# Kernel tuning notes

Measured on AMD Instinct MI355X. Metric: run time of the kernel, lower is better.

The kernel has to match this reference:

```python
import jax, jax.numpy as jnp
import numpy as np

B, NQ, NK = 4, 2048, 2048
QDIM = CDIM = 1024
H, DH = 16, 64  # heads, dim_head; inner_dim = H*DH = 1024
SCALE = DH ** -0.5
WSTD = 0.02


def setup_inputs() -> dict:
    key = jax.random.key(0)
    ks = jax.random.split(key, 6)
    inner = H * DH
    return {
        "x": jax.random.normal(ks[0], (B, NQ, QDIM), dtype=jnp.float32),
        "context": jax.random.normal(ks[1], (B, NK, CDIM), dtype=jnp.float32),
        "Wq": jax.random.normal(ks[2], (inner, QDIM), dtype=jnp.float32) * WSTD,
        "Wk": jax.random.normal(ks[3], (inner, CDIM), dtype=jnp.float32) * WSTD,
        "Wv": jax.random.normal(ks[4], (inner, CDIM), dtype=jnp.float32) * WSTD,
        "Wo": jax.random.normal(ks[5], (QDIM, inner), dtype=jnp.float32) * WSTD,
        "bo": jnp.zeros((QDIM,), dtype=jnp.float32),
    }


def reference(x, context, Wq, Wk, Wv, Wo, bo):
    b, nq, _ = x.shape
    nk = context.shape[1]
    # Linear projections (torch Linear: y = x @ W.T)
    q = (x @ Wq.T).reshape(b, nq, H, DH)        # b n h d
    k = (context @ Wk.T).reshape(b, nk, H, DH)
    v = (context @ Wv.T).reshape(b, nk, H, DH)
    # sim = Q K^T * scale, materialized as in the original einsum
    sim = jnp.einsum('bihd,bjhd->bhij', q, k) * SCALE
    attn = jax.nn.softmax(sim, axis=-1)
    out = jnp.einsum('bhij,bjhd->bihd', attn, v).reshape(b, nq, H * DH)
    return out @ Wo.T + bo
```

## Files before the change

### kernel.cpp

```cpp
#include <hip/hip_runtime.h>
#include <cstdint>
#include <cstddef>


typedef __attribute__((ext_vector_type(8))) short short8;
typedef __attribute__((ext_vector_type(4))) float f32x4;
typedef __attribute__((ext_vector_type(4))) unsigned short ushort4v;

#define GLD16(gsrc, ldst) \
  __builtin_amdgcn_global_load_lds((const __attribute__((address_space(1))) unsigned int*)(gsrc), \
                                   (__attribute__((address_space(3))) unsigned int*)(ldst), 16, 0, 0)

__device__ __forceinline__ unsigned short f32_to_bf16(float f) {
  unsigned int u = __builtin_bit_cast(unsigned int, f);
  u += 0x7FFFu + ((u >> 16) & 1u);
  return (unsigned short)(u >> 16);
}

__device__ __forceinline__ unsigned int pack2_bf16(float lo, float hi) {
  return (unsigned int)f32_to_bf16(lo) | ((unsigned int)f32_to_bf16(hi) << 16);
}

__global__ __launch_bounds__(256) void cvt_bf16(const float* __restrict__ in,
                                                unsigned short* __restrict__ out,
                                                int n4, float scale) {
  int i = blockIdx.x * 256 + threadIdx.x;
  const int stride = gridDim.x * 256;
  for (; i < n4; i += stride) {
    float4 v = reinterpret_cast<const float4*>(in)[i];
    ushort4v o;
    o.x = f32_to_bf16(v.x * scale);
    o.y = f32_to_bf16(v.y * scale);
    o.z = f32_to_bf16(v.z * scale);
    o.w = f32_to_bf16(v.w * scale);
    reinterpret_cast<ushort4v*>(out)[i] = o;
  }
}

template<bool BF16_OUT, bool BIAS>
__global__ __launch_bounds__(256) void gemm_bt(const unsigned short* __restrict__ A,
                                               const unsigned short* __restrict__ Bm,
                                               void* __restrict__ Cout,
                                               const float* __restrict__ bias,
                                               int M, int N, int K) {
  __shared__ __align__(16) unsigned short smA[128 * 32];
  __shared__ __align__(16) unsigned short smB[128 * 32];

  const int t    = threadIdx.x;
  const int lane = t & 63;
  const int wid  = t >> 6;
  const int l15  = lane & 15;
  const int l16  = lane >> 4;
  const int m0   = blockIdx.y * 128;
  const int n0   = blockIdx.x * 128;
  const int wr   = (wid >> 1) * 64;
  const int wc   = (wid & 1) * 64;

  f32x4 acc[4][4];
#pragma unroll
  for (int i = 0; i < 4; ++i)
#pragma unroll
    for (int j = 0; j < 4; ++j) acc[i][j] = (f32x4){0.f, 0.f, 0.f, 0.f};

  const char* Abase = (const char*)A + (size_t)m0 * K * 2;
  const char* Bbase = (const char*)Bm + (size_t)n0 * K * 2;

  for (int k0 = 0; k0 < K; k0 += 32) {
#pragma unroll
    for (int i = 0; i < 2; ++i) {
      int g = i * 256 + t;
      int r = g >> 2, c = g & 3;
      int cs = c ^ ((r >> 1) & 3);
      const char* srcA = Abase + (size_t)r * (K * 2) + (size_t)k0 * 2 + cs * 16;
      const char* srcB = Bbase + (size_t)r * (K * 2) + (size_t)k0 * 2 + cs * 16;
      char* dA = (char*)smA + (g & ~63) * 16;
      char* dB = (char*)smB + (g & ~63) * 16;
      GLD16(srcA, dA);
      GLD16(srcB, dB);
    }
    __syncthreads();

    short8 af[4], bfv[4];
#pragma unroll
    for (int mi = 0; mi < 4; ++mi) {
      int row = wr + mi * 16 + l15;
      int cs = l16 ^ ((row >> 1) & 3);
      af[mi] = *reinterpret_cast<const short8*>((const char*)smA + row * 64 + cs * 16);
    }
#pragma unroll
    for (int ni = 0; ni < 4; ++ni) {
      int row = wc + ni * 16 + l15;
      int cs = l16 ^ ((row >> 1) & 3);
      bfv[ni] = *reinterpret_cast<const short8*>((const char*)smB + row * 64 + cs * 16);
    }
#pragma unroll
    for (int mi = 0; mi < 4; ++mi)
#pragma unroll
      for (int ni = 0; ni < 4; ++ni)
        acc[mi][ni] = __builtin_amdgcn_mfma_f32_16x16x32_bf16(af[mi], bfv[ni], acc[mi][ni], 0, 0, 0);
    __syncthreads();
  }

#pragma unroll
  for (int mi = 0; mi < 4; ++mi)
#pragma unroll
    for (int ni = 0; ni < 4; ++ni)
#pragma unroll
      for (int r = 0; r < 4; ++r) {
        int row = m0 + wr + mi * 16 + l16 * 4 + r;
        int col = n0 + wc + ni * 16 + l15;
        float v = acc[mi][ni][r];
        if (BIAS) v += bias[col];
        if (BF16_OUT)
          ((unsigned short*)Cout)[(size_t)row * N + col] = f32_to_bf16(v);
        else
          ((float*)Cout)[(size_t)row * N + col] = v;
      }
}

__global__ __launch_bounds__(256, 3) void flash_attn(const unsigned short* __restrict__ Q,
                                                     const unsigned short* __restrict__ Kb,
                                                     const unsigned short* __restrict__ Vt,
                                                     unsigned short* __restrict__ O) {
  __shared__ __align__(16) unsigned short smK[2][64 * 64];
  __shared__ __align__(16) unsigned short smV[2][64 * 64];
  __shared__ __align__(16) unsigned int   smP[4][32 * 36];

  const int t    = threadIdx.x;
  const int lane = t & 63;
  const int wid  = t >> 6;
  const int l15  = lane & 15;
  const int l16  = lane >> 4;
  const int qt   = blockIdx.x;
  const int h    = blockIdx.y;
  const int b    = blockIdx.z;

  const char* Kbase = (const char*)Kb + ((size_t)(b * 2048) * 1024 + h * 64) * 2;
  const char* Vbase = (const char*)Vt + ((size_t)(h * 64) * 8192 + b * 2048) * 2;
  unsigned int* smPw = &smP[wid][0];

  short8 qf[2][2];
#pragma unroll
  for (int qg = 0; qg < 2; ++qg)
#pragma unroll
    for (int kk = 0; kk < 2; ++kk) {
      size_t idx = (size_t)(b * 2048 + qt * 128 + wid * 32 + qg * 16 + l15) * 1024
                 + (size_t)h * 64 + kk * 32 + l16 * 8;
      qf[qg][kk] = *reinterpret_cast<const short8*>(&Q[idx]);
    }
  asm volatile("s_waitcnt vmcnt(0)" ::: "memory");
  __builtin_amdgcn_sched_barrier(0);

  auto stage = [&](int buf, int j0) {
#pragma unroll
    for (int i = 0; i < 2; ++i) {
      int g = i * 256 + t;
      int r = g >> 3, c = g & 7;
      int cs = c ^ (r & 7);
      const char* srcK = Kbase + (size_t)(j0 + r) * 2048 + cs * 16;
      const char* srcV = Vbase + (size_t)r * 16384 + (size_t)j0 * 2 + cs * 16;
      GLD16(srcK, (char*)&smK[buf][0] + (g & ~63) * 16);
      GLD16(srcV, (char*)&smV[buf][0] + (g & ~63) * 16);
    }
  };

  f32x4 accO[2][4];
  float m_run[2], l_run[2];
#pragma unroll
  for (int qg = 0; qg < 2; ++qg) {
    m_run[qg] = -1.0e30f;
    l_run[qg] = 0.f;
#pragma unroll
    for (int di = 0; di < 4; ++di) accO[qg][di] = (f32x4){0.f, 0.f, 0.f, 0.f};
  }

  stage(0, 0);

  for (int jt = 0; jt < 32; ++jt) {
    const int buf = jt & 1;
    if (jt < 31) {
      stage(buf ^ 1, (jt + 1) * 64);
      asm volatile("s_waitcnt vmcnt(4)" ::: "memory");
    } else {
      asm volatile("s_waitcnt vmcnt(0)" ::: "memory");
    }
    __builtin_amdgcn_sched_barrier(0);
    __builtin_amdgcn_s_barrier();

    short8 kf[4][2];
#pragma unroll
    for (int kc = 0; kc < 4; ++kc)
#pragma unroll
      for (int kk = 0; kk < 2; ++kk) {
        int row = kc * 16 + l15;
        int cs = (kk * 4 + l16) ^ (row & 7);
        kf[kc][kk] = *reinterpret_cast<const short8*>((const char*)&smK[buf][0] + row * 128 + cs * 16);
      }
    f32x4 s[2][4];
    const f32x4 z = (f32x4){0.f, 0.f, 0.f, 0.f};
    __builtin_amdgcn_s_setprio(1);
#pragma unroll
    for (int qg = 0; qg < 2; ++qg)
#pragma unroll
      for (int kc = 0; kc < 4; ++kc) {
        f32x4 tmp = __builtin_amdgcn_mfma_f32_16x16x32_bf16(kf[kc][0], qf[qg][0], z, 0, 0, 0);
        s[qg][kc] = __builtin_amdgcn_mfma_f32_16x16x32_bf16(kf[kc][1], qf[qg][1], tmp, 0, 0, 0);
      }
    __builtin_amdgcn_s_setprio(0);

    short8 vf[4][2];
#pragma unroll
    for (int di = 0; di < 4; ++di)
#pragma unroll
      for (int kk = 0; kk < 2; ++kk) {
        int row = di * 16 + l15;
        int cs = (kk * 4 + l16) ^ (row & 7);
        vf[di][kk] = *reinterpret_cast<const short8*>((const char*)&smV[buf][0] + row * 128 + cs * 16);
      }

#pragma unroll
    for (int qg = 0; qg < 2; ++qg) {
      float vmax = s[qg][0][0];
#pragma unroll
      for (int kc = 0; kc < 4; ++kc)
#pragma unroll
        for (int r = 0; r < 4; ++r) vmax = fmaxf(vmax, s[qg][kc][r]);
      vmax = fmaxf(vmax, __shfl_xor(vmax, 16));
      vmax = fmaxf(vmax, __shfl_xor(vmax, 32));

      if (__any(vmax > m_run[qg] + 8.0f)) {
        float mnew = fmaxf(m_run[qg], vmax);
        float alpha = __expf(m_run[qg] - mnew);
        m_run[qg] = mnew;
        l_run[qg] *= alpha;
        int av = __builtin_bit_cast(int, alpha);
#pragma unroll
        for (int r = 0; r < 4; ++r) {
          float at = __builtin_bit_cast(float, __builtin_amdgcn_ds_bpermute((l16 * 4 + r) * 4, av));
#pragma unroll
          for (int di = 0; di < 4; ++di) accO[qg][di][r] *= at;
        }
      }

      float rsum = 0.f;
#pragma unroll
      for (int kc = 0; kc < 4; ++kc)
#pragma unroll
        for (int r = 0; r < 4; ++r) {
          float p = __expf(s[qg][kc][r] - m_run[qg]);
          s[qg][kc][r] = p;
          rsum += p;
        }
      rsum += __shfl_xor(rsum, 16);
      rsum += __shfl_xor(rsum, 32);
      l_run[qg] += rsum;

#pragma unroll
      for (int kc = 0; kc < 4; ++kc) {
        unsigned int w0 = pack2_bf16(s[qg][kc][0], s[qg][kc][1]);
        unsigned int w1 = pack2_bf16(s[qg][kc][2], s[qg][kc][3]);
        int word = (qg * 16 + l15) * 36 + kc * 8 + l16 * 2;
        *reinterpret_cast<uint2*>(&smPw[word]) = uint2{w0, w1};
      }
    }

    asm volatile("s_waitcnt lgkmcnt(0)" ::: "memory");
    __builtin_amdgcn_sched_barrier(0);

    short8 pf[2][2];
#pragma unroll
    for (int qg = 0; qg < 2; ++qg)
#pragma unroll
      for (int kk = 0; kk < 2; ++kk) {
        int word = (qg * 16 + l15) * 36 + kk * 16 + l16 * 4;
        pf[qg][kk] = *reinterpret_cast<const short8*>(&smPw[word]);
      }

    __builtin_amdgcn_s_setprio(1);
#pragma unroll
    for (int qg = 0; qg < 2; ++qg)
#pragma unroll
      for (int di = 0; di < 4; ++di) {
        accO[qg][di] = __builtin_amdgcn_mfma_f32_16x16x32_bf16(pf[qg][0], vf[di][0], accO[qg][di], 0, 0, 0);
        accO[qg][di] = __builtin_amdgcn_mfma_f32_16x16x32_bf16(pf[qg][1], vf[di][1], accO[qg][di], 0, 0, 0);
      }
    __builtin_amdgcn_s_setprio(0);

    __builtin_amdgcn_s_barrier();
  }

#pragma unroll
  for (int qg = 0; qg < 2; ++qg) {
    float inv = 1.f / l_run[qg];
    int iv = __builtin_bit_cast(int, inv);
#pragma unroll
    for (int r = 0; r < 4; ++r) {
      float it = __builtin_bit_cast(float, __builtin_amdgcn_ds_bpermute((l16 * 4 + r) * 4, iv));
      int row = b * 2048 + qt * 128 + wid * 32 + qg * 16 + l16 * 4 + r;
#pragma unroll
      for (int di = 0; di < 4; ++di) {
        int col = h * 64 + di * 16 + l15;
        O[(size_t)row * 1024 + col] = f32_to_bf16(accO[qg][di][r] * it);
      }
    }
  }
}

extern "C" void kernel_launch(void* const* d_in, const int* in_sizes, int n_in,
                              void* d_out, int out_size, void* d_ws, size_t ws_size,
                              hipStream_t stream) {
  (void)in_sizes; (void)n_in; (void)out_size; (void)ws_size;
  const float* x   = (const float*)d_in[0];
  const float* ctx = (const float*)d_in[1];
  const float* Wq  = (const float*)d_in[2];
  const float* Wk  = (const float*)d_in[3];
  const float* Wv  = (const float*)d_in[4];
  const float* Wo  = (const float*)d_in[5];
  const float* bo  = (const float*)d_in[6];
  float* out = (float*)d_out;

  char* ws = (char*)d_ws;
  const size_t MB = 1024 * 1024;
  unsigned short* xb  = (unsigned short*)(ws + 0);
  unsigned short* cb  = (unsigned short*)(ws + 16 * MB);
  unsigned short* Qb  = (unsigned short*)(ws + 32 * MB);
  unsigned short* Kb  = (unsigned short*)(ws + 48 * MB);
  unsigned short* Vtb = (unsigned short*)(ws + 64 * MB);
  unsigned short* wqb = (unsigned short*)(ws + 80 * MB);
  unsigned short* wkb = (unsigned short*)(ws + 82 * MB);
  unsigned short* wvb = (unsigned short*)(ws + 84 * MB);
  unsigned short* wob = (unsigned short*)(ws + 86 * MB);
  unsigned short* Ob  = xb;

  const float SCALE = 0.125f;

  cvt_bf16<<<2048, 256, 0, stream>>>(x,   xb,  (4*2048*1024)/4, 1.0f);
  cvt_bf16<<<2048, 256, 0, stream>>>(ctx, cb,  (4*2048*1024)/4, 1.0f);
  cvt_bf16<<<1024, 256, 0, stream>>>(Wq,  wqb, (1024*1024)/4, SCALE);
  cvt_bf16<<<1024, 256, 0, stream>>>(Wk,  wkb, (1024*1024)/4, 1.0f);
  cvt_bf16<<<1024, 256, 0, stream>>>(Wv,  wvb, (1024*1024)/4, 1.0f);
  cvt_bf16<<<1024, 256, 0, stream>>>(Wo,  wob, (1024*1024)/4, 1.0f);

  gemm_bt<true, false><<<dim3(1024/128, 8192/128), 256, 0, stream>>>(xb, wqb, Qb, nullptr, 8192, 1024, 1024);
  gemm_bt<true, false><<<dim3(1024/128, 8192/128), 256, 0, stream>>>(cb, wkb, Kb, nullptr, 8192, 1024, 1024);
  gemm_bt<true, false><<<dim3(8192/128, 1024/128), 256, 0, stream>>>(wvb, cb, Vtb, nullptr, 1024, 8192, 1024);

  flash_attn<<<dim3(2048/128, 16, 4), 256, 0, stream>>>(Qb, Kb, Vtb, Ob);

  gemm_bt<false, true><<<dim3(1024/128, 8192/128), 256, 0, stream>>>(Ob, wob, out, bo, 8192, 1024, 1024);
}
```

Baseline: 382.6 us.

## Double-buffer GEMM LDS, use exp2 softmax, merge weight conversions

The GEMM now double-buffers its LDS tiles, prefetching the next K slice while the current one runs MFMAs. The flash-attention loop is reordered so the next K/V stage issues before compute and is waited on at the end of each iteration. Separately, log2(e) is folded into the Q weight scale so softmax can use the hardware exp2, with a rescale threshold retuned to match. P packing uses the native v_cvt_pk_bf16_f32 instruction, and the four weight conversions are merged into one launch. Costs are more LDS per GEMM block, which may lower occupancy, and a looser lazy-rescale threshold that slightly raises overflow risk.

```diff
diff --git a/kernel.cpp b/kernel.cpp
--- a/kernel.cpp
+++ b/kernel.cpp
@@ -17,8 +17,18 @@
   return (unsigned short)(u >> 16);
 }
 
-__device__ __forceinline__ unsigned int pack2_bf16(float lo, float hi) {
-  return (unsigned int)f32_to_bf16(lo) | ((unsigned int)f32_to_bf16(hi) << 16);
+__device__ __forceinline__ unsigned int cvtpk_bf16(float lo, float hi) {
+  unsigned int r;
+  asm("v_cvt_pk_bf16_f32 %0, %1, %2" : "=v"(r) : "v"(lo), "v"(hi));
+  return r;
+}
+
+__device__ __forceinline__ float exp2_fast(float x) {
+#if __has_builtin(__builtin_amdgcn_exp2f)
+  return __builtin_amdgcn_exp2f(x);
+#else
+  return exp2f(x);
+#endif
 }
 
 __global__ __launch_bounds__(256) void cvt_bf16(const float* __restrict__ in,
@@ -37,14 +47,37 @@
   }
 }
 
+__global__ __launch_bounds__(256) void cvt_w4(const float* __restrict__ a, const float* __restrict__ b,
+                                              const float* __restrict__ c, const float* __restrict__ d,
+                                              unsigned short* __restrict__ oa, unsigned short* __restrict__ ob,
+                                              unsigned short* __restrict__ oc, unsigned short* __restrict__ od,
+                                              float scale_a) {
+  int seg = blockIdx.x >> 8;
+  int blk = blockIdx.x & 255;
+  const float* in = seg == 0 ? a : seg == 1 ? b : seg == 2 ? c : d;
+  unsigned short* out = seg == 0 ? oa : seg == 1 ? ob : seg == 2 ? oc : od;
+  float sc = seg == 0 ? scale_a : 1.0f;
+  int i = blk * 256 + threadIdx.x;
+#pragma unroll
+  for (int k = 0; k < 4; ++k, i += 65536) {
+    float4 v = reinterpret_cast<const float4*>(in)[i];
+    ushort4v o;
+    o.x = f32_to_bf16(v.x * sc);
+    o.y = f32_to_bf16(v.y * sc);
+    o.z = f32_to_bf16(v.z * sc);
+    o.w = f32_to_bf16(v.w * sc);
+    reinterpret_cast<ushort4v*>(out)[i] = o;
+  }
+}
+
 template<bool BF16_OUT, bool BIAS>
 __global__ __launch_bounds__(256) void gemm_bt(const unsigned short* __restrict__ A,
                                                const unsigned short* __restrict__ Bm,
                                                void* __restrict__ Cout,
                                                const float* __restrict__ bias,
                                                int M, int N, int K) {
-  __shared__ __align__(16) unsigned short smA[128 * 32];
-  __shared__ __align__(16) unsigned short smB[128 * 32];
+  __shared__ __align__(16) unsigned short smA[2][128 * 32];
+  __shared__ __align__(16) unsigned short smB[2][128 * 32];
 
   const int t    = threadIdx.x;
   const int lane = t & 63;
@@ -65,40 +98,51 @@
   const char* Abase = (const char*)A + (size_t)m0 * K * 2;
   const char* Bbase = (const char*)Bm + (size_t)n0 * K * 2;
 
-  for (int k0 = 0; k0 < K; k0 += 32) {
+  auto stageG = [&](int bufi, int k0) {
 #pragma unroll
     for (int i = 0; i < 2; ++i) {
       int g = i * 256 + t;
       int r = g >> 2, c = g & 3;
       int cs = c ^ ((r >> 1) & 3);
-      const char* srcA = Abase + (size_t)r * (K * 2) + (size_t)k0 * 2 + cs * 16;
-      const char* srcB = Bbase + (size_t)r * (K * 2) + (size_t)k0 * 2 + cs * 16;
-      char* dA = (char*)smA + (g & ~63) * 16;
-      char* dB = (char*)smB + (g & ~63) * 16;
-      GLD16(srcA, dA);
-      GLD16(srcB, dB);
-    }
-    __syncthreads();
+      GLD16(Abase + (size_t)r * (K * 2) + (size_t)k0 * 2 + cs * 16,
+            (char*)&smA[bufi][0] + (g & ~63) * 16);
+      GLD16(Bbase + (size_t)r * (K * 2) + (size_t)k0 * 2 + cs * 16,
+            (char*)&smB[bufi][0] + (g & ~63) * 16);
+    }
+  };
+
+  const int nk = K >> 5;
+  stageG(0, 0);
+  asm volatile("s_waitcnt vmcnt(0)" ::: "memory");
+  __builtin_amdgcn_s_barrier();
+
+  for (int t0 = 0; t0 < nk; ++t0) {
+    const int bufi = t0 & 1;
+    if (t0 + 1 < nk) stageG(bufi ^ 1, (t0 + 1) * 32);
 
     short8 af[4], bfv[4];
 #pragma unroll
     for (int mi = 0; mi < 4; ++mi) {
       int row = wr + mi * 16 + l15;
       int cs = l16 ^ ((row >> 1) & 3);
-      af[mi] = *reinterpret_cast<const short8*>((const char*)smA + row * 64 + cs * 16);
+      af[mi] = *reinterpret_cast<const short8*>((const char*)&smA[bufi][0] + row * 64 + cs * 16);
     }
 #pragma unroll
     for (int ni = 0; ni < 4; ++ni) {
       int row = wc + ni * 16 + l15;
       int cs = l16 ^ ((row >> 1) & 3);
-      bfv[ni] = *reinterpret_cast<const short8*>((const char*)smB + row * 64 + cs * 16);
-    }
+      bfv[ni] = *reinterpret_cast<const short8*>((const char*)&smB[bufi][0] + row * 64 + cs * 16);
+    }
+    __builtin_amdgcn_s_setprio(1);
 #pragma unroll
     for (int mi = 0; mi < 4; ++mi)
 #pragma unroll
       for (int ni = 0; ni < 4; ++ni)
         acc[mi][ni] = __builtin_amdgcn_mfma_f32_16x16x32_bf16(af[mi], bfv[ni], acc[mi][ni], 0, 0, 0);
-    __syncthreads();
+    __builtin_amdgcn_s_setprio(0);
+
+    asm volatile("s_waitcnt vmcnt(0)" ::: "memory");
+    __builtin_amdgcn_s_barrier();
   }
 
 #pragma unroll
@@ -139,18 +183,6 @@
   const char* Vbase = (const char*)Vt + ((size_t)(h * 64) * 8192 + b * 2048) * 2;
   unsigned int* smPw = &smP[wid][0];
 
-  short8 qf[2][2];
-#pragma unroll
-  for (int qg = 0; qg < 2; ++qg)
-#pragma unroll
-    for (int kk = 0; kk < 2; ++kk) {
-      size_t idx = (size_t)(b * 2048 + qt * 128 + wid * 32 + qg * 16 + l15) * 1024
-                 + (size_t)h * 64 + kk * 32 + l16 * 8;
-      qf[qg][kk] = *reinterpret_cast<const short8*>(&Q[idx]);
-    }
-  asm volatile("s_waitcnt vmcnt(0)" ::: "memory");
-  __builtin_amdgcn_sched_barrier(0);
-
   auto stage = [&](int buf, int j0) {
 #pragma unroll
     for (int i = 0; i < 2; ++i) {
@@ -164,6 +196,18 @@
     }
   };
 
+  stage(0, 0);
+
+  short8 qf[2][2];
+#pragma unroll
+  for (int qg = 0; qg < 2; ++qg)
+#pragma unroll
+    for (int kk = 0; kk < 2; ++kk) {
+      size_t idx = (size_t)(b * 2048 + qt * 128 + wid * 32 + qg * 16 + l15) * 1024
+                 + (size_t)h * 64 + kk * 32 + l16 * 8;
+      qf[qg][kk] = *reinterpret_cast<const short8*>(&Q[idx]);
+    }
+
   f32x4 accO[2][4];
   float m_run[2], l_run[2];
 #pragma unroll
@@ -174,18 +218,12 @@
     for (int di = 0; di < 4; ++di) accO[qg][di] = (f32x4){0.f, 0.f, 0.f, 0.f};
   }
 
-  stage(0, 0);
+  asm volatile("s_waitcnt vmcnt(0)" ::: "memory");
+  __builtin_amdgcn_s_barrier();
 
   for (int jt = 0; jt < 32; ++jt) {
     const int buf = jt & 1;
-    if (jt < 31) {
-      stage(buf ^ 1, (jt + 1) * 64);
-      asm volatile("s_waitcnt vmcnt(4)" ::: "memory");
-    } else {
-      asm volatile("s_waitcnt vmcnt(0)" ::: "memory");
-    }
-    __builtin_amdgcn_sched_barrier(0);
-    __builtin_amdgcn_s_barrier();
+    if (jt < 31) stage(buf ^ 1, (jt + 1) * 64);
 
     short8 kf[4][2];
 #pragma unroll
@@ -228,9 +266,9 @@
       vmax = fmaxf(vmax, __shfl_xor(vmax, 16));
       vmax = fmaxf(vmax, __shfl_xor(vmax, 32));
 
-      if (__any(vmax > m_run[qg] + 8.0f)) {
+      if (__any(vmax > m_run[qg] + 11.5f)) {
         float mnew = fmaxf(m_run[qg], vmax);
-        float alpha = __expf(m_run[qg] - mnew);
+        float alpha = exp2_fast(m_run[qg] - mnew);
         m_run[qg] = mnew;
         l_run[qg] *= alpha;
         int av = __builtin_bit_cast(int, alpha);
@@ -247,7 +285,7 @@
       for (int kc = 0; kc < 4; ++kc)
 #pragma unroll
         for (int r = 0; r < 4; ++r) {
-          float p = __expf(s[qg][kc][r] - m_run[qg]);
+          float p = exp2_fast(s[qg][kc][r] - m_run[qg]);
           s[qg][kc][r] = p;
           rsum += p;
         }
@@ -257,8 +295,8 @@
 
 #pragma unroll
       for (int kc = 0; kc < 4; ++kc) {
-        unsigned int w0 = pack2_bf16(s[qg][kc][0], s[qg][kc][1]);
-        unsigned int w1 = pack2_bf16(s[qg][kc][2], s[qg][kc][3]);
+        unsigned int w0 = cvtpk_bf16(s[qg][kc][0], s[qg][kc][1]);
+        unsigned int w1 = cvtpk_bf16(s[qg][kc][2], s[qg][kc][3]);
         int word = (qg * 16 + l15) * 36 + kc * 8 + l16 * 2;
         *reinterpret_cast<uint2*>(&smPw[word]) = uint2{w0, w1};
       }
@@ -286,6 +324,7 @@
       }
     __builtin_amdgcn_s_setprio(0);
 
+    asm volatile("s_waitcnt vmcnt(0)" ::: "memory");
     __builtin_amdgcn_s_barrier();
   }
 
@@ -332,14 +371,11 @@
   unsigned short* wob = (unsigned short*)(ws + 86 * MB);
   unsigned short* Ob  = xb;
 
-  const float SCALE = 0.125f;
-
-  cvt_bf16<<<2048, 256, 0, stream>>>(x,   xb,  (4*2048*1024)/4, 1.0f);
-  cvt_bf16<<<2048, 256, 0, stream>>>(ctx, cb,  (4*2048*1024)/4, 1.0f);
-  cvt_bf16<<<1024, 256, 0, stream>>>(Wq,  wqb, (1024*1024)/4, SCALE);
-  cvt_bf16<<<1024, 256, 0, stream>>>(Wk,  wkb, (1024*1024)/4, 1.0f);
-  cvt_bf16<<<1024, 256, 0, stream>>>(Wv,  wvb, (1024*1024)/4, 1.0f);
-  cvt_bf16<<<1024, 256, 0, stream>>>(Wo,  wob, (1024*1024)/4, 1.0f);
+  const float SCALE_LOG2E = 0.125f * 1.4426950408889634f;
+
+  cvt_bf16<<<2048, 256, 0, stream>>>(x,   xb, (4*2048*1024)/4, 1.0f);
+  cvt_bf16<<<2048, 256, 0, stream>>>(ctx, cb, (4*2048*1024)/4, 1.0f);
+  cvt_w4<<<1024, 256, 0, stream>>>(Wq, Wk, Wv, Wo, wqb, wkb, wvb, wob, SCALE_LOG2E);
 
   gemm_bt<true, false><<<dim3(1024/128, 8192/128), 256, 0, stream>>>(xb, wqb, Qb, nullptr, 8192, 1024, 1024);
   gemm_bt<true, false><<<dim3(1024/128, 8192/128), 256, 0, stream>>>(cb, wkb, Kb, nullptr, 8192, 1024, 1024);
```

Result: faster. 355.2 us (-7.2%).
